# Performance work log

Measured on AMD Instinct MI355X. Metric: run time of the kernel, lower is better.

The kernel has to match this reference:

```python
import jax, jax.numpy as jnp
import numpy as np

N = 3072      # nodes
D = 256       # embed_dim
H = 8         # heads
E = 98304     # edges (avg degree 32)
B = 16        # graphs in batch


def setup_inputs() -> dict:
    key = jax.random.key(0)
    ks = jax.random.split(key, 14)
    w = lambda k, sh: jax.random.normal(k, sh, jnp.float32) * 0.02
    return {
        "x": jax.random.normal(ks[0], (N, D), jnp.float32),
        "edge_attr": jax.random.normal(ks[1], (E, 4), jnp.float32),
        "Wq": w(ks[2], (D, D)), "bq": jnp.zeros((D,), jnp.float32),
        "Wk": w(ks[3], (D, D)), "bk": jnp.zeros((D,), jnp.float32),
        "Wv": w(ks[4], (D, D)), "bv": jnp.zeros((D,), jnp.float32),
        "Wo": w(ks[5], (D, D)), "bo": jnp.zeros((D,), jnp.float32),
        "We": w(ks[6], (4, H)), "be": jnp.zeros((H,), jnp.float32),
        "edge_index": jax.random.randint(ks[7], (2, E), 0, N),
        "batch": jnp.sort(jax.random.randint(ks[8], (N,), 0, B)),
    }


def reference(x, edge_attr, Wq, bq, Wk, bk, Wv, bv, Wo, bo, We, be,
              edge_index, batch):
    n, d = x.shape
    h = be.shape[0]
    hd = d // h
    # projections -> [h, n, hd]
    Q = (x @ Wq + bq).reshape(n, h, hd).transpose(1, 0, 2)
    K = (x @ Wk + bk).reshape(n, h, hd).transpose(1, 0, 2)
    V = (x @ Wv + bv).reshape(n, h, hd).transpose(1, 0, 2)
    # dense attention scores [h, n, n]
    scores = jnp.einsum('hnd,hmd->hnm', Q, K) / np.float32(np.sqrt(hd))
    # per-edge bias scatter-add (accumulate over duplicate edges)
    edge_bias = edge_attr @ We + be                     # [E, h]
    scores = scores.at[:, edge_index[0], edge_index[1]].add(edge_bias.T)
    # block-diagonal batch mask
    same_graph = batch[:, None] == batch[None, :]       # [n, n]
    scores = jnp.where(same_graph[None], scores, -jnp.inf)
    attn = jax.nn.softmax(scores, axis=-1)              # dropout: eval mode (identity)
    out = jnp.einsum('hnm,hmd->hnd', attn, V)           # [h, n, hd]
    out = out.transpose(1, 0, 2).reshape(n, d)
    return out @ Wo + bo
```

## Files before the change

kernel.cpp:

```cpp
#include <hip/hip_runtime.h>
#include <hip/hip_bf16.h>
#include <math.h>

#define N_NODES 3072
#define NPAD    3104
#define DIM     256
#define NH      8
#define HD      32
#define E_EDGES 98304
#define B_GRAPHS 16
#define RCAP    96
#define MAXC    332
#define PSTR    260
#define TR      16
#define SCALE   0.17677669529663689f

typedef __attribute__((ext_vector_type(8))) short bf16x8;
typedef __attribute__((ext_vector_type(4))) float f32x4;
typedef __attribute__((ext_vector_type(4))) unsigned short ushort4v;

__device__ inline unsigned short f2b(float f) {
    __hip_bfloat16 h = __float2bfloat16(f);
    return *reinterpret_cast<unsigned short*>(&h);
}
__device__ inline float b2f(unsigned short u) {
    __hip_bfloat16 h = *reinterpret_cast<__hip_bfloat16*>(&u);
    return __bfloat162float(h);
}


__device__ inline void xsplit_body(int u, int t, const float* __restrict__ x,
                                   unsigned short* __restrict__ xh,
                                   unsigned short* __restrict__ xl) {
    const int gid = u * 256 + t;
    float4 v = ((const float4*)x)[gid];
    ushort4v h, l;
    float c[4] = {v.x, v.y, v.z, v.w};
    #pragma unroll
    for (int i = 0; i < 4; ++i) {
        unsigned short hi = f2b(c[i]);
        h[i] = hi;
        l[i] = f2b(c[i] - b2f(hi));
    }
    ((ushort4v*)xh)[gid] = h;
    ((ushort4v*)xl)[gid] = l;
}

__device__ inline void wtrans_body(int wb, int t,
                                   const float* __restrict__ Wq, const float* __restrict__ Wk,
                                   const float* __restrict__ Wv, const float* __restrict__ Wo,
                                   unsigned short* __restrict__ Wth,
                                   unsigned short* __restrict__ Wtl,
                                   float (*tile)[33]) {
    const int mat = wb >> 6, tidx = wb & 63;
    const int tk = (tidx >> 3) * 32, tn = (tidx & 7) * 32;
    const float* W = (mat == 0) ? Wq : (mat == 1) ? Wk : (mat == 2) ? Wv : Wo;
    const int kk = t >> 5, nn = t & 31;
    #pragma unroll
    for (int p = 0; p < 4; ++p)
        tile[nn][kk + p * 8] = W[(size_t)(tk + kk + p * 8) * DIM + tn + nn];
    __syncthreads();
    const int n = t >> 3, kq = (t & 7) * 4;
    ushort4v h, l;
    #pragma unroll
    for (int i = 0; i < 4; ++i) {
        float v = tile[n][kq + i];
        unsigned short hi = f2b(v);
        h[i] = hi;
        l[i] = f2b(v - b2f(hi));
    }
    size_t o = (size_t)mat * DIM * DIM + (size_t)(tn + n) * DIM + tk + kq;
    *(ushort4v*)(Wth + o) = h;
    *(ushort4v*)(Wtl + o) = l;
}

__device__ inline void vtpad_body(int i, const int* __restrict__ batch,
                                  unsigned short* __restrict__ VT,
                                  int* __restrict__ gstart) {
    VT[(size_t)(i >> 5) * NPAD + N_NODES + (i & 31)] = 0;
    if (i < N_NODES) {
        int bb = batch[i];
        int bp = (i == 0) ? -1 : batch[i - 1];
        for (int g = bp + 1; g <= bb; ++g) gstart[g] = i;
        if (i == N_NODES - 1)
            for (int g = bb + 1; g <= B_GRAPHS; ++g) gstart[g] = N_NODES;
    }
}

__device__ inline void edge_body(int e, const float* __restrict__ ea,
                                 const float* __restrict__ We, const float* __restrict__ be,
                                 const int* __restrict__ erow, const int* __restrict__ ecolin,
                                 float* __restrict__ ebias, int* __restrict__ tcur,
                                 unsigned int* __restrict__ tbuck) {
    const int row = erow[e];
    const int col = ecolin[e];
    int pos = atomicAdd(&tcur[row], 1);
    if (pos < RCAP)
        tbuck[(size_t)row * RCAP + pos] = ((unsigned int)e << 12) | (unsigned int)col;
    float4 a = ((const float4*)ea)[e];
    #pragma unroll
    for (int h = 0; h < NH; ++h) {
        float bb = fmaf(a.x, We[0 * NH + h],
                   fmaf(a.y, We[1 * NH + h],
                   fmaf(a.z, We[2 * NH + h],
                   fmaf(a.w, We[3 * NH + h], be[h]))));
        ebias[(size_t)h * E_EDGES + e] = bb;
    }
}

__device__ inline void qkv_body(int u, int t,
                                const unsigned short* __restrict__ xh, const unsigned short* __restrict__ xl,
                                const unsigned short* __restrict__ Wth, const unsigned short* __restrict__ Wtl,
                                const float* __restrict__ bq, const float* __restrict__ bk,
                                const float* __restrict__ bv,
                                unsigned short* __restrict__ Qb, unsigned short* __restrict__ Kb,
                                unsigned short* __restrict__ VT) {
    const int w = t >> 6, lane = t & 63;
    const int l16 = lane & 15, lq = lane >> 4;
    const int bx = u % 96, by = u / 96;
    const int mat = by >> 2;
    const int rb = bx * 32 + (w & 1) * 16;
    const int nb = (by & 3) * 64 + (w >> 1) * 32;
    const unsigned short* Wh = Wth + (size_t)mat * DIM * DIM;
    const unsigned short* Wl = Wtl + (size_t)mat * DIM * DIM;

    f32x4 acc[2] = {{0,0,0,0},{0,0,0,0}};

    if (mat < 2) {
        const size_t arow = (size_t)(rb + l16) * DIM + (lq << 3);
        #pragma unroll
        for (int kc = 0; kc < 8; ++kc) {
            const int k = kc * 32;
            bf16x8 ah = *(const bf16x8*)(xh + arow + k);
            bf16x8 al = *(const bf16x8*)(xl + arow + k);
            #pragma unroll
            for (int ct = 0; ct < 2; ++ct) {
                const size_t bo_ = (size_t)(nb + ct * 16 + l16) * DIM + k + (lq << 3);
                bf16x8 bh = *(const bf16x8*)(Wh + bo_);
                bf16x8 bl = *(const bf16x8*)(Wl + bo_);
                acc[ct] = __builtin_amdgcn_mfma_f32_16x16x32_bf16(ah, bh, acc[ct], 0, 0, 0);
                acc[ct] = __builtin_amdgcn_mfma_f32_16x16x32_bf16(ah, bl, acc[ct], 0, 0, 0);
                acc[ct] = __builtin_amdgcn_mfma_f32_16x16x32_bf16(al, bh, acc[ct], 0, 0, 0);
            }
        }
        const float* bias = (mat == 0) ? bq : bk;
        unsigned short* outp = (mat == 0) ? Qb : Kb;
        #pragma unroll
        for (int ct = 0; ct < 2; ++ct) {
            const int n = nb + ct * 16 + l16;
            const float bvl = bias[n];
            #pragma unroll
            for (int r = 0; r < 4; ++r)
                outp[(size_t)(rb + lq * 4 + r) * DIM + n] = f2b(acc[ct][r] + bvl);
        }
    } else {
        const size_t brow = (size_t)(rb + l16) * DIM + (lq << 3);
        #pragma unroll
        for (int kc = 0; kc < 8; ++kc) {
            const int k = kc * 32;
            bf16x8 bxh = *(const bf16x8*)(xh + brow + k);
            bf16x8 bxl = *(const bf16x8*)(xl + brow + k);
            #pragma unroll
            for (int ct = 0; ct < 2; ++ct) {
                const size_t ao_ = (size_t)(nb + ct * 16 + l16) * DIM + k + (lq << 3);
                bf16x8 awh = *(const bf16x8*)(Wh + ao_);
                bf16x8 awl = *(const bf16x8*)(Wl + ao_);
                acc[ct] = __builtin_amdgcn_mfma_f32_16x16x32_bf16(awh, bxh, acc[ct], 0, 0, 0);
                acc[ct] = __builtin_amdgcn_mfma_f32_16x16x32_bf16(awh, bxl, acc[ct], 0, 0, 0);
                acc[ct] = __builtin_amdgcn_mfma_f32_16x16x32_bf16(awl, bxh, acc[ct], 0, 0, 0);
            }
        }
        #pragma unroll
        for (int ct = 0; ct < 2; ++ct) {
            #pragma unroll
            for (int r = 0; r < 4; ++r) {
                const int ncol = nb + ct * 16 + lq * 4 + r;
                VT[(size_t)ncol * NPAD + rb + l16] = f2b(acc[ct][r] + bv[ncol]);
            }
        }
    }
}

__device__ inline void attn_head(int h, int row0, int nrows, int gs,
                                 int ncols, int ags, int coff, int tcols, int cpad,
                                 int t,
                                 const unsigned short* __restrict__ Qb,
                                 const unsigned short* __restrict__ Kb,
                                 const unsigned short* __restrict__ VT,
                                 const int* __restrict__ tcur,
                                 const unsigned int* __restrict__ tbuck,
                                 const float* __restrict__ ebias,
                                 float (*s)[MAXC], float* rowinv,
                                 float (*pre)[PSTR]) {
    const int wave = t >> 6, lane = t & 63;
    const int l16 = lane & 15, lq = lane >> 4;

    {
        int arow = min(row0 + l16, N_NODES - 1);
        const bf16x8 aq = *(const bf16x8*)(Qb + (size_t)arow * DIM + h * HD + (lq << 3));
        const int nchunk16 = (tcols + 15) >> 4;
        for (int j = wave; j < nchunk16; j += 4) {
            const int c0 = j << 4;
            int krow = min(ags + c0 + l16, N_NODES - 1);
            bf16x8 bk = *(const bf16x8*)(Kb + (size_t)krow * DIM + h * HD + (lq << 3));
            f32x4 d = {0.f, 0.f, 0.f, 0.f};
            d = __builtin_amdgcn_mfma_f32_16x16x32_bf16(aq, bk, d, 0, 0, 0);
            const int col = c0 + l16, rbase = lq * 4;
            #pragma unroll
            for (int r = 0; r < 4; ++r) s[rbase + r][col] = d[r] * SCALE;
        }
    }
    __syncthreads();

    {
        const int r = t >> 4, sub = t & 15;
        if (r < nrows) {
            const int cnt = min(tcur[row0 + r], RCAP);
            const unsigned int* bk = tbuck + (size_t)(row0 + r) * RCAP;
            for (int idx = sub; idx < cnt; idx += 16) {
                unsigned int p = bk[idx];
                int c = (int)(p & 0xFFFu) - gs;
                if (c >= 0 && c < ncols)
                    atomicAdd(&s[r][coff + c], ebias[(size_t)h * E_EDGES + (p >> 12)]);
            }
        }
    }
    __syncthreads();

    {
        const int r = t >> 4, sub = t & 15;
        if (r < nrows) {
            float m = -INFINITY;
            for (int c = coff + sub; c < tcols; c += 16) m = fmaxf(m, s[r][c]);
            m = fmaxf(m, __shfl_xor(m, 1, 16));
            m = fmaxf(m, __shfl_xor(m, 2, 16));
            m = fmaxf(m, __shfl_xor(m, 4, 16));
            m = fmaxf(m, __shfl_xor(m, 8, 16));
            float sum = 0.f;
            for (int c = sub; c < cpad; c += 16) {
                float e = 0.f;
                if (c >= coff && c < tcols) e = __expf(s[r][c] - m);
                sum += e;
                s[r][c] = e;
            }
            sum += __shfl_xor(sum, 1, 16);
            sum += __shfl_xor(sum, 2, 16);
            sum += __shfl_xor(sum, 4, 16);
            sum += __shfl_xor(sum, 8, 16);
            if (sub == 0) rowinv[r] = 1.0f / sum;
        } else {
            for (int c = sub; c < cpad; c += 16) s[r][c] = 0.f;
        }
    }
    __syncthreads();

    f32x4 o = {0.f, 0.f, 0.f, 0.f};
    {
        const int half = wave >> 1, par = wave & 1;
        const int kout = l16 + (half << 4);
        const int nchunk32 = cpad >> 5;
        const unsigned short* vrow = VT + (size_t)(h * HD + kout) * NPAD + ags + (lq << 3);
        for (int j = par; j < nchunk32; j += 2) {
            const int c0 = j << 5;
            const float4 p0 = *(const float4*)&s[l16][c0 + (lq << 3)];
            const float4 p1 = *(const float4*)&s[l16][c0 + (lq << 3) + 4];
            bf16x8 ap;
            ap[0] = f2b(p0.x); ap[1] = f2b(p0.y); ap[2] = f2b(p0.z); ap[3] = f2b(p0.w);
            ap[4] = f2b(p1.x); ap[5] = f2b(p1.y); ap[6] = f2b(p1.z); ap[7] = f2b(p1.w);
            bf16x8 bv = *(const bf16x8*)(vrow + c0);
            o = __builtin_amdgcn_mfma_f32_16x16x32_bf16(ap, bv, o, 0, 0, 0);
        }
    }
    __syncthreads();
    {
        float* red = &s[0][0];
        const int rbase = lq * 4;
        #pragma unroll
        for (int r = 0; r < 4; ++r)
            red[((wave << 4) + rbase + r) * 17 + l16] = o[r];
    }
    __syncthreads();
    {
        const int row = t >> 4, kl = t & 15;
        if (row < nrows) {
            float* red = &s[0][0];
            float v0 = red[(row) * 17 + kl]        + red[(16 + row) * 17 + kl];
            float v1 = red[(32 + row) * 17 + kl]   + red[(48 + row) * 17 + kl];
            float sc = rowinv[row];
            pre[row][h * HD + kl]      = v0 * sc;
            pre[row][h * HD + 16 + kl] = v1 * sc;
        }
    }
}

__global__ __launch_bounds__(256) void prep_a(
    const float* __restrict__ x,
    const float* __restrict__ Wq, const float* __restrict__ Wk,
    const float* __restrict__ Wv, const float* __restrict__ Wo,
    unsigned short* __restrict__ xh, unsigned short* __restrict__ xl,
    unsigned short* __restrict__ Wth, unsigned short* __restrict__ Wtl,
    int* __restrict__ tcur)
{
    __shared__ float tile[32][33];
    const int b = blockIdx.x, t = threadIdx.x;
    if (b < 768)        xsplit_body(b, t, x, xh, xl);
    else if (b < 1024)  wtrans_body(b - 768, t, Wq, Wk, Wv, Wo, Wth, Wtl, tile);
    else                tcur[(b - 1024) * 256 + t] = 0;
}

__global__ __launch_bounds__(256) void stage2(
    const unsigned short* __restrict__ xh, const unsigned short* __restrict__ xl,
    const unsigned short* __restrict__ Wth, const unsigned short* __restrict__ Wtl,
    const float* __restrict__ bq, const float* __restrict__ bk,
    const float* __restrict__ bv,
    const float* __restrict__ ea, const float* __restrict__ We,
    const float* __restrict__ be,
    const int* __restrict__ erow, const int* __restrict__ ecolin,
    const int* __restrict__ batch,
    unsigned short* __restrict__ Qb, unsigned short* __restrict__ Kb,
    unsigned short* __restrict__ VT,
    float* __restrict__ ebias, int* __restrict__ gstart,
    int* __restrict__ tcur, unsigned int* __restrict__ tbuck)
{
    const int b = blockIdx.x, t = threadIdx.x;
    if (b < 384)        edge_body(b * 256 + t, ea, We, be, erow, ecolin, ebias, tcur, tbuck);
    else if (b < 1536)  qkv_body(b - 384, t, xh, xl, Wth, Wtl, bq, bk, bv, Qb, Kb, VT);
    else                vtpad_body((b - 1536) * 256 + t, batch, VT, gstart);
}

__global__ __launch_bounds__(256) void attn_out(
    const unsigned short* __restrict__ Qb, const unsigned short* __restrict__ Kb,
    const unsigned short* __restrict__ VT,
    const int* __restrict__ gstart,
    const int* __restrict__ tcur, const unsigned int* __restrict__ tbuck,
    const float* __restrict__ ebias,
    const unsigned short* __restrict__ Wth, const unsigned short* __restrict__ Wtl,
    const float* __restrict__ bo, float* __restrict__ out)
{
    __shared__ __align__(16) float s[TR][MAXC];
    __shared__ __align__(16) float pre[TR][PSTR];
    __shared__ float rowinv[TR];

    const int g = blockIdx.x, tile_ = blockIdx.y;
    const int gs = gstart[g], ge = gstart[g + 1];
    const int row0 = gs + tile_ * TR;
    if (row0 >= ge) return;
    const int nrows = min(TR, ge - row0);
    const int ncols = ge - gs;
    const int ags   = gs & ~15;
    const int coff  = gs - ags;
    const int tcols = coff + ncols;
    const int cpad  = (tcols + 31) & ~31;
    const int t = threadIdx.x;

    for (int h = 0; h < NH; ++h) {
        attn_head(h, row0, nrows, gs, ncols, ags, coff, tcols, cpad, t,
                  Qb, Kb, VT, tcur, tbuck, ebias, s, rowinv, pre);
        __syncthreads();
    }

    for (int i = t; i < (TR - nrows) * 256; i += 256)
        pre[nrows + (i >> 8)][i & 255] = 0.f;
    __syncthreads();

    const int w = t >> 6, lane = t & 63;
    const int l16 = lane & 15, lq = lane >> 4;
    const unsigned short* Wh = Wth + (size_t)3 * DIM * DIM;
    const unsigned short* Wl = Wtl + (size_t)3 * DIM * DIM;

    f32x4 acc[4] = {{0,0,0,0},{0,0,0,0},{0,0,0,0},{0,0,0,0}};
    #pragma unroll
    for (int kc = 0; kc < 8; ++kc) {
        const int k = kc * 32;
        const float4 a0 = *(const float4*)&pre[l16][k + (lq << 3)];
        const float4 a1 = *(const float4*)&pre[l16][k + (lq << 3) + 4];
        bf16x8 ah, al;
        ah[0] = f2b(a0.x); al[0] = f2b(a0.x - b2f(ah[0]));
        ah[1] = f2b(a0.y); al[1] = f2b(a0.y - b2f(ah[1]));
        ah[2] = f2b(a0.z); al[2] = f2b(a0.z - b2f(ah[2]));
        ah[3] = f2b(a0.w); al[3] = f2b(a0.w - b2f(ah[3]));
        ah[4] = f2b(a1.x); al[4] = f2b(a1.x - b2f(ah[4]));
        ah[5] = f2b(a1.y); al[5] = f2b(a1.y - b2f(ah[5]));
        ah[6] = f2b(a1.z); al[6] = f2b(a1.z - b2f(ah[6]));
        ah[7] = f2b(a1.w); al[7] = f2b(a1.w - b2f(ah[7]));
        #pragma unroll
        for (int ct = 0; ct < 4; ++ct) {
            const size_t bo_ = (size_t)(w * 64 + ct * 16 + l16) * DIM + k + (lq << 3);
            bf16x8 bh = *(const bf16x8*)(Wh + bo_);
            bf16x8 bl = *(const bf16x8*)(Wl + bo_);
            acc[ct] = __builtin_amdgcn_mfma_f32_16x16x32_bf16(ah, bh, acc[ct], 0, 0, 0);
            acc[ct] = __builtin_amdgcn_mfma_f32_16x16x32_bf16(ah, bl, acc[ct], 0, 0, 0);
            acc[ct] = __builtin_amdgcn_mfma_f32_16x16x32_bf16(al, bh, acc[ct], 0, 0, 0);
        }
    }
    #pragma unroll
    for (int ct = 0; ct < 4; ++ct) {
        const int n = w * 64 + ct * 16 + l16;
        const float bvl = bo[n];
        #pragma unroll
        for (int r = 0; r < 4; ++r) {
            const int rr = lq * 4 + r;
            if (rr < nrows)
                out[(size_t)(row0 + rr) * DIM + n] = acc[ct][r] + bvl;
        }
    }
}

extern "C" void kernel_launch(void* const* d_in, const int* in_sizes, int n_in,
                              void* d_out, int out_size, void* d_ws, size_t ws_size,
                              hipStream_t stream) {
    const float* x   = (const float*)d_in[0];
    const float* ea  = (const float*)d_in[1];
    const float* Wq  = (const float*)d_in[2];  const float* bq = (const float*)d_in[3];
    const float* Wk  = (const float*)d_in[4];  const float* bk = (const float*)d_in[5];
    const float* Wv  = (const float*)d_in[6];  const float* bv = (const float*)d_in[7];
    const float* Wo  = (const float*)d_in[8];  const float* bo = (const float*)d_in[9];
    const float* We  = (const float*)d_in[10]; const float* be = (const float*)d_in[11];
    const int*   eidx  = (const int*)d_in[12];
    const int*   batch = (const int*)d_in[13];
    const int* erow   = eidx;
    const int* ecolin = eidx + E_EDGES;

    const size_t ND = (size_t)N_NODES * DIM;
    const size_t WD = (size_t)DIM * DIM;

    unsigned short* Qb   = (unsigned short*)d_ws;
    unsigned short* Kb   = Qb + ND;
    unsigned short* VT   = Kb + ND;
    unsigned short* xh   = VT + (size_t)DIM * NPAD;
    unsigned short* xl   = xh + ND;
    unsigned short* Wth  = xl + ND;
    unsigned short* Wtl  = Wth + 4 * WD;
    unsigned int* tbuck  = (unsigned int*)(Wtl + 4 * WD);
    float* ebias  = (float*)(tbuck + (size_t)N_NODES * RCAP);
    int* tcur     = (int*)(ebias + (size_t)NH * E_EDGES);
    int* gstart   = tcur + N_NODES;

    prep_a<<<dim3(1036), dim3(256), 0, stream>>>(x, Wq, Wk, Wv, Wo,
                                                 xh, xl, Wth, Wtl, tcur);
    stage2<<<dim3(1568), dim3(256), 0, stream>>>(xh, xl, Wth, Wtl, bq, bk, bv,
                                                 ea, We, be, erow, ecolin, batch,
                                                 Qb, Kb, VT, ebias, gstart, tcur, tbuck);
    attn_out<<<dim3(B_GRAPHS, 24), dim3(256), 0, stream>>>(Qb, Kb, VT, gstart,
                                                           tcur, tbuck, ebias,
                                                           Wth, Wtl, bo, (float*)d_out);
}
```

Measured before the change: 184.4 us.

## Split attention across heads in grid, last-arriving block does output projection

The attention kernel now launches one block per (graph, row tile, head) instead of looping over the 8 heads inside a block. Per-head results go to a global scratch buffer, and an atomic counter per tile lets the last of the 8 head blocks run the Wo projection. Edge bias is now computed on the fly from edge_attr inside the attention kernel rather than precomputed into an ebias array in stage2. The aim is 8x more blocks for better occupancy and less precompute traffic, at the cost of a global round trip for the pre-projection data and atomic or fence overhead.

```diff
diff --git a/kernel.cpp b/kernel.cpp
--- a/kernel.cpp
+++ b/kernel.cpp
@@ -11,8 +11,8 @@
 #define B_GRAPHS 16
 #define RCAP    96
 #define MAXC    332
-#define PSTR    260
 #define TR      16
+#define NTILE   24
 #define SCALE   0.17677669529663689f
 
 typedef __attribute__((ext_vector_type(8))) short bf16x8;
@@ -87,25 +87,14 @@
     }
 }
 
-__device__ inline void edge_body(int e, const float* __restrict__ ea,
-                                 const float* __restrict__ We, const float* __restrict__ be,
+__device__ inline void edge_body(int e,
                                  const int* __restrict__ erow, const int* __restrict__ ecolin,
-                                 float* __restrict__ ebias, int* __restrict__ tcur,
-                                 unsigned int* __restrict__ tbuck) {
+                                 int* __restrict__ tcur, unsigned int* __restrict__ tbuck) {
     const int row = erow[e];
     const int col = ecolin[e];
     int pos = atomicAdd(&tcur[row], 1);
     if (pos < RCAP)
         tbuck[(size_t)row * RCAP + pos] = ((unsigned int)e << 12) | (unsigned int)col;
-    float4 a = ((const float4*)ea)[e];
-    #pragma unroll
-    for (int h = 0; h < NH; ++h) {
-        float bb = fmaf(a.x, We[0 * NH + h],
-                   fmaf(a.y, We[1 * NH + h],
-                   fmaf(a.z, We[2 * NH + h],
-                   fmaf(a.w, We[3 * NH + h], be[h]))));
-        ebias[(size_t)h * E_EDGES + e] = bb;
-    }
 }
 
 __device__ inline void qkv_body(int u, int t,
@@ -181,19 +170,75 @@
     }
 }
 
-__device__ inline void attn_head(int h, int row0, int nrows, int gs,
-                                 int ncols, int ags, int coff, int tcols, int cpad,
-                                 int t,
-                                 const unsigned short* __restrict__ Qb,
-                                 const unsigned short* __restrict__ Kb,
-                                 const unsigned short* __restrict__ VT,
-                                 const int* __restrict__ tcur,
-                                 const unsigned int* __restrict__ tbuck,
-                                 const float* __restrict__ ebias,
-                                 float (*s)[MAXC], float* rowinv,
-                                 float (*pre)[PSTR]) {
+__global__ __launch_bounds__(256) void prep_a(
+    const float* __restrict__ x,
+    const float* __restrict__ Wq, const float* __restrict__ Wk,
+    const float* __restrict__ Wv, const float* __restrict__ Wo,
+    unsigned short* __restrict__ xh, unsigned short* __restrict__ xl,
+    unsigned short* __restrict__ Wth, unsigned short* __restrict__ Wtl,
+    int* __restrict__ tcur, unsigned int* __restrict__ pcnt)
+{
+    __shared__ float tile[32][33];
+    const int b = blockIdx.x, t = threadIdx.x;
+    if (b < 768)        xsplit_body(b, t, x, xh, xl);
+    else if (b < 1024)  wtrans_body(b - 768, t, Wq, Wk, Wv, Wo, Wth, Wtl, tile);
+    else {
+        const int i = (b - 1024) * 256 + t;
+        if (i < N_NODES)                tcur[i] = 0;
+        else if (i < N_NODES + B_GRAPHS * NTILE) pcnt[i - N_NODES] = 0u;
+    }
+}
+
+__global__ __launch_bounds__(256) void stage2(
+    const unsigned short* __restrict__ xh, const unsigned short* __restrict__ xl,
+    const unsigned short* __restrict__ Wth, const unsigned short* __restrict__ Wtl,
+    const float* __restrict__ bq, const float* __restrict__ bk,
+    const float* __restrict__ bv,
+    const int* __restrict__ erow, const int* __restrict__ ecolin,
+    const int* __restrict__ batch,
+    unsigned short* __restrict__ Qb, unsigned short* __restrict__ Kb,
+    unsigned short* __restrict__ VT,
+    int* __restrict__ gstart, int* __restrict__ tcur, unsigned int* __restrict__ tbuck)
+{
+    const int b = blockIdx.x, t = threadIdx.x;
+    if (b < 384)        edge_body(b * 256 + t, erow, ecolin, tcur, tbuck);
+    else if (b < 1536)  qkv_body(b - 384, t, xh, xl, Wth, Wtl, bq, bk, bv, Qb, Kb, VT);
+    else                vtpad_body((b - 1536) * 256 + t, batch, VT, gstart);
+}
+
+__global__ __launch_bounds__(256) void attn_go(
+    const unsigned short* __restrict__ Qb, const unsigned short* __restrict__ Kb,
+    const unsigned short* __restrict__ VT,
+    const int* __restrict__ gstart,
+    const int* __restrict__ tcur, const unsigned int* __restrict__ tbuck,
+    const float* __restrict__ ea, const float* __restrict__ We,
+    const float* __restrict__ be,
+    const unsigned short* __restrict__ Wth, const unsigned short* __restrict__ Wtl,
+    const float* __restrict__ bo,
+    float* __restrict__ pre, unsigned int* __restrict__ pcnt,
+    float* __restrict__ out)
+{
+    __shared__ __align__(16) float s[TR][MAXC];
+    __shared__ float rowinv[TR];
+    __shared__ int isLast;
+
+    const int g = blockIdx.x, tile_ = blockIdx.y, h = blockIdx.z;
+    const int gs = gstart[g], ge = gstart[g + 1];
+    const int row0 = gs + tile_ * TR;
+    if (row0 >= ge) return;
+    const int nrows = min(TR, ge - row0);
+    const int ncols = ge - gs;
+    const int ags   = gs & ~15;
+    const int coff  = gs - ags;
+    const int tcols = coff + ncols;
+    const int cpad  = (tcols + 31) & ~31;
+    const int t = threadIdx.x;
     const int wave = t >> 6, lane = t & 63;
     const int l16 = lane & 15, lq = lane >> 4;
+
+    const float we0 = We[0 * NH + h], we1 = We[1 * NH + h];
+    const float we2 = We[2 * NH + h], we3 = We[3 * NH + h];
+    const float beh = be[h];
 
     {
         int arow = min(row0 + l16, N_NODES - 1);
@@ -220,8 +265,12 @@
             for (int idx = sub; idx < cnt; idx += 16) {
                 unsigned int p = bk[idx];
                 int c = (int)(p & 0xFFFu) - gs;
-                if (c >= 0 && c < ncols)
-                    atomicAdd(&s[r][coff + c], ebias[(size_t)h * E_EDGES + (p >> 12)]);
+                if (c >= 0 && c < ncols) {
+                    float4 a = ((const float4*)ea)[p >> 12];
+                    float bb = fmaf(a.x, we0, fmaf(a.y, we1,
+                               fmaf(a.z, we2, fmaf(a.w, we3, beh))));
+                    atomicAdd(&s[r][coff + c], bb);
+                }
             }
         }
     }
@@ -287,121 +336,64 @@
             float v0 = red[(row) * 17 + kl]        + red[(16 + row) * 17 + kl];
             float v1 = red[(32 + row) * 17 + kl]   + red[(48 + row) * 17 + kl];
             float sc = rowinv[row];
-            pre[row][h * HD + kl]      = v0 * sc;
-            pre[row][h * HD + 16 + kl] = v1 * sc;
-        }
-    }
-}
-
-__global__ __launch_bounds__(256) void prep_a(
-    const float* __restrict__ x,
-    const float* __restrict__ Wq, const float* __restrict__ Wk,
-    const float* __restrict__ Wv, const float* __restrict__ Wo,
-    unsigned short* __restrict__ xh, unsigned short* __restrict__ xl,
-    unsigned short* __restrict__ Wth, unsigned short* __restrict__ Wtl,
-    int* __restrict__ tcur)
-{
-    __shared__ float tile[32][33];
-    const int b = blockIdx.x, t = threadIdx.x;
-    if (b < 768)        xsplit_body(b, t, x, xh, xl);
-    else if (b < 1024)  wtrans_body(b - 768, t, Wq, Wk, Wv, Wo, Wth, Wtl, tile);
-    else                tcur[(b - 1024) * 256 + t] = 0;
-}
-
-__global__ __launch_bounds__(256) void stage2(
-    const unsigned short* __restrict__ xh, const unsigned short* __restrict__ xl,
-    const unsigned short* __restrict__ Wth, const unsigned short* __restrict__ Wtl,
-    const float* __restrict__ bq, const float* __restrict__ bk,
-    const float* __restrict__ bv,
-    const float* __restrict__ ea, const float* __restrict__ We,
-    const float* __restrict__ be,
-    const int* __restrict__ erow, const int* __restrict__ ecolin,
-    const int* __restrict__ batch,
-    unsigned short* __restrict__ Qb, unsigned short* __restrict__ Kb,
-    unsigned short* __restrict__ VT,
-    float* __restrict__ ebias, int* __restrict__ gstart,
-    int* __restrict__ tcur, unsigned int* __restrict__ tbuck)
-{
-    const int b = blockIdx.x, t = threadIdx.x;
-    if (b < 384)        edge_body(b * 256 + t, ea, We, be, erow, ecolin, ebias, tcur, tbuck);
-    else if (b < 1536)  qkv_body(b - 384, t, xh, xl, Wth, Wtl, bq, bk, bv, Qb, Kb, VT);
-    else                vtpad_body((b - 1536) * 256 + t, batch, VT, gstart);
-}
-
-__global__ __launch_bounds__(256) void attn_out(
-    const unsigned short* __restrict__ Qb, const unsigned short* __restrict__ Kb,
-    const unsigned short* __restrict__ VT,
-    const int* __restrict__ gstart,
-    const int* __restrict__ tcur, const unsigned int* __restrict__ tbuck,
-    const float* __restrict__ ebias,
-    const unsigned short* __restrict__ Wth, const unsigned short* __restrict__ Wtl,
-    const float* __restrict__ bo, float* __restrict__ out)
-{
-    __shared__ __align__(16) float s[TR][MAXC];
-    __shared__ __align__(16) float pre[TR][PSTR];
-    __shared__ float rowinv[TR];
-
-    const int g = blockIdx.x, tile_ = blockIdx.y;
-    const int gs = gstart[g], ge = gstart[g + 1];
-    const int row0 = gs + tile_ * TR;
-    if (row0 >= ge) return;
-    const int nrows = min(TR, ge - row0);
-    const int ncols = ge - gs;
-    const int ags   = gs & ~15;
-    const int coff  = gs - ags;
-    const int tcols = coff + ncols;
-    const int cpad  = (tcols + 31) & ~31;
-    const int t = threadIdx.x;
-
-    for (int h = 0; h < NH; ++h) {
-        attn_head(h, row0, nrows, gs, ncols, ags, coff, tcols, cpad, t,
-                  Qb, Kb, VT, tcur, tbuck, ebias, s, rowinv, pre);
-        __syncthreads();
-    }
-
-    for (int i = t; i < (TR - nrows) * 256; i += 256)
-        pre[nrows + (i >> 8)][i & 255] = 0.f;
-    __syncthreads();
-
-    const int w = t >> 6, lane = t & 63;
-    const int l16 = lane & 15, lq = lane >> 4;
-    const unsigned short* Wh = Wth + (size_t)3 * DIM * DIM;
-    const unsigned short* Wl = Wtl + (size_t)3 * DIM * DIM;
-
-    f32x4 acc[4] = {{0,0,0,0},{0,0,0,0},{0,0,0,0},{0,0,0,0}};
-    #pragma unroll
-    for (int kc = 0; kc < 8; ++kc) {
-        const int k = kc * 32;
-        const float4 a0 = *(const float4*)&pre[l16][k + (lq << 3)];
-        const float4 a1 = *(const float4*)&pre[l16][k + (lq << 3) + 4];
-        bf16x8 ah, al;
-        ah[0] = f2b(a0.x); al[0] = f2b(a0.x - b2f(ah[0]));
-        ah[1] = f2b(a0.y); al[1] = f2b(a0.y - b2f(ah[1]));
-        ah[2] = f2b(a0.z); al[2] = f2b(a0.z - b2f(ah[2]));
-        ah[3] = f2b(a0.w); al[3] = f2b(a0.w - b2f(ah[3]));
-        ah[4] = f2b(a1.x); al[4] = f2b(a1.x - b2f(ah[4]));
-        ah[5] = f2b(a1.y); al[5] = f2b(a1.y - b2f(ah[5]));
-        ah[6] = f2b(a1.z); al[6] = f2b(a1.z - b2f(ah[6]));
-        ah[7] = f2b(a1.w); al[7] = f2b(a1.w - b2f(ah[7]));
+            size_t ob = (size_t)(row0 + row) * DIM + h * HD;
+            pre[ob + kl]      = v0 * sc;
+            pre[ob + 16 + kl] = v1 * sc;
+        }
+    }
+
+    __threadfence();
+    __syncthreads();
+    if (t == 0) {
+        unsigned old = __hip_atomic_fetch_add(&pcnt[g * NTILE + tile_], 1u,
+                                              __ATOMIC_ACQ_REL, __HIP_MEMORY_SCOPE_AGENT);
+        isLast = (old == NH - 1);
+    }
+    __syncthreads();
+    if (!isLast) return;
+    __threadfence();
+
+    {
+        const int w = wave;
+        const unsigned short* Wh = Wth + (size_t)3 * DIM * DIM;
+        const unsigned short* Wl = Wtl + (size_t)3 * DIM * DIM;
+        const size_t arow = (size_t)(row0 + l16) * DIM + (lq << 3);
+
+        f32x4 acc[4] = {{0,0,0,0},{0,0,0,0},{0,0,0,0},{0,0,0,0}};
+        #pragma unroll
+        for (int kc = 0; kc < 8; ++kc) {
+            const int k = kc * 32;
+            const float4 a0 = *(const float4*)&pre[arow + k];
+            const float4 a1 = *(const float4*)&pre[arow + k + 4];
+            bf16x8 ah, al;
+            ah[0] = f2b(a0.x); al[0] = f2b(a0.x - b2f(ah[0]));
+            ah[1] = f2b(a0.y); al[1] = f2b(a0.y - b2f(ah[1]));
+            ah[2] = f2b(a0.z); al[2] = f2b(a0.z - b2f(ah[2]));
+            ah[3] = f2b(a0.w); al[3] = f2b(a0.w - b2f(ah[3]));
+            ah[4] = f2b(a1.x); al[4] = f2b(a1.x - b2f(ah[4]));
+            ah[5] = f2b(a1.y); al[5] = f2b(a1.y - b2f(ah[5]));
+            ah[6] = f2b(a1.z); al[6] = f2b(a1.z - b2f(ah[6]));
+            ah[7] = f2b(a1.w); al[7] = f2b(a1.w - b2f(ah[7]));
+            #pragma unroll
+            for (int ct = 0; ct < 4; ++ct) {
+                const size_t bo_ = (size_t)(w * 64 + ct * 16 + l16) * DIM + k + (lq << 3);
+                bf16x8 bh = *(const bf16x8*)(Wh + bo_);
+                bf16x8 bl = *(const bf16x8*)(Wl + bo_);
+                acc[ct] = __builtin_amdgcn_mfma_f32_16x16x32_bf16(ah, bh, acc[ct], 0, 0, 0);
+                acc[ct] = __builtin_amdgcn_mfma_f32_16x16x32_bf16(ah, bl, acc[ct], 0, 0, 0);
+                acc[ct] = __builtin_amdgcn_mfma_f32_16x16x32_bf16(al, bh, acc[ct], 0, 0, 0);
+            }
+        }
         #pragma unroll
         for (int ct = 0; ct < 4; ++ct) {
-            const size_t bo_ = (size_t)(w * 64 + ct * 16 + l16) * DIM + k + (lq << 3);
-            bf16x8 bh = *(const bf16x8*)(Wh + bo_);
-            bf16x8 bl = *(const bf16x8*)(Wl + bo_);
-            acc[ct] = __builtin_amdgcn_mfma_f32_16x16x32_bf16(ah, bh, acc[ct], 0, 0, 0);
-            acc[ct] = __builtin_amdgcn_mfma_f32_16x16x32_bf16(ah, bl, acc[ct], 0, 0, 0);
-            acc[ct] = __builtin_amdgcn_mfma_f32_16x16x32_bf16(al, bh, acc[ct], 0, 0, 0);
-        }
-    }
-    #pragma unroll
-    for (int ct = 0; ct < 4; ++ct) {
-        const int n = w * 64 + ct * 16 + l16;
-        const float bvl = bo[n];
-        #pragma unroll
-        for (int r = 0; r < 4; ++r) {
-            const int rr = lq * 4 + r;
-            if (rr < nrows)
-                out[(size_t)(row0 + rr) * DIM + n] = acc[ct][r] + bvl;
+            const int n = w * 64 + ct * 16 + l16;
+            const float bvl = bo[n];
+            #pragma unroll
+            for (int r = 0; r < 4; ++r) {
+                const int rr = lq * 4 + r;
+                if (rr < nrows)
+                    out[(size_t)(row0 + rr) * DIM + n] = acc[ct][r] + bvl;
+            }
         }
     }
 }
@@ -432,16 +424,17 @@
     unsigned short* Wth  = xl + ND;
     unsigned short* Wtl  = Wth + 4 * WD;
     unsigned int* tbuck  = (unsigned int*)(Wtl + 4 * WD);
-    float* ebias  = (float*)(tbuck + (size_t)N_NODES * RCAP);
-    int* tcur     = (int*)(ebias + (size_t)NH * E_EDGES);
-    int* gstart   = tcur + N_NODES;
-
-    prep_a<<<dim3(1036), dim3(256), 0, stream>>>(x, Wq, Wk, Wv, Wo,
-                                                 xh, xl, Wth, Wtl, tcur);
+    float* pre    = (float*)(tbuck + (size_t)N_NODES * RCAP);
+    int* tcur     = (int*)(pre + ND);
+    unsigned int* pcnt = (unsigned int*)(tcur + N_NODES);
+    int* gstart   = (int*)(pcnt + B_GRAPHS * NTILE);
+
+    prep_a<<<dim3(1038), dim3(256), 0, stream>>>(x, Wq, Wk, Wv, Wo,
+                                                 xh, xl, Wth, Wtl, tcur, pcnt);
     stage2<<<dim3(1568), dim3(256), 0, stream>>>(xh, xl, Wth, Wtl, bq, bk, bv,
-                                                 ea, We, be, erow, ecolin, batch,
-                                                 Qb, Kb, VT, ebias, gstart, tcur, tbuck);
-    attn_out<<<dim3(B_GRAPHS, 24), dim3(256), 0, stream>>>(Qb, Kb, VT, gstart,
-                                                           tcur, tbuck, ebias,
-                                                           Wth, Wtl, bo, (float*)d_out);
-}
+                                                 erow, ecolin, batch,
+                                                 Qb, Kb, VT, gstart, tcur, tbuck);
+    attn_go<<<dim3(B_GRAPHS, NTILE, NH), dim3(256), 0, stream>>>(
+        Qb, Kb, VT, gstart, tcur, tbuck, ea, We, be,
+        Wth, Wtl, bo, pre, pcnt, (float*)d_out);
+}
```

Measured after the change: 332.4 us. 1.8x slower.
